# Optimization experiments

Hardware: AMD Instinct MI355X
Metric: run time of the kernel (lower is better)

The kernel has to match this reference:

```python
import jax, jax.numpy as jnp
import numpy as np

IN_F = 4096
OUT_F = 4096
R = 128
E = 8            # expert_num
R_PER = R // E   # per-expert low rank (16)
ALPHA = 16
SCALING = ALPHA / R
N = 8192


def setup_inputs() -> dict:
    key = jax.random.key(0)
    k_x, k_w0, k_g, k_a, k_b = jax.random.split(key, 5)
    x = jax.random.normal(k_x, (N, IN_F), dtype=jnp.float32)
    W0 = jax.random.normal(k_w0, (OUT_F, IN_F), dtype=jnp.float32) * 0.02   # base_layer weight
    Wg = jax.random.normal(k_g, (E, IN_F), dtype=jnp.float32) * 0.02        # GateL weight
    A = jax.random.normal(k_a, (E, R_PER, IN_F), dtype=jnp.float32) * 0.01  # stacked loraA weights
    B = jax.random.normal(k_b, (E, OUT_F, R_PER), dtype=jnp.float32) * 0.01 # stacked loraB weights
    return {"x": x, "W0": W0, "Wg": Wg, "A": A, "B": B}


def reference(x, W0, Wg, A, B):
    # base layer: result = x @ W0^T
    result = jnp.einsum('nd,od->no', x, W0)
    # gate: softmax over experts (dim=1 for 2D input)
    gate = jax.nn.softmax(jnp.einsum('nd,ed->ne', x, Wg), axis=1)  # [N, E]
    # per-expert low-rank: h_i = x @ A_i^T ; y_i = h_i @ B_i^T
    h = jnp.einsum('nd,erd->ner', x, A)        # [N, E, R_PER]
    y = jnp.einsum('ner,eor->neo', h, B)       # [N, E, OUT_F]
    lora = jnp.einsum('neo,ne->no', y, gate)   # gated weighted sum over experts
    return result + SCALING * lora
```

## Files before the change

kernel.cpp:

```cpp
#include <hip/hip_runtime.h>
#include <hip/hip_bf16.h>

#define IN_F   4096
#define OUT_F  4096
#define RTOT   128
#define NE     8
#define RP     16
#define NROWS  8192
#define KC     (IN_F + RTOT)
#define NG     144
#define SCALING 0.125f
#define KSPLIT 4

typedef __attribute__((ext_vector_type(8))) short bf16x8;
typedef __attribute__((ext_vector_type(4))) float f32x4;

__device__ __forceinline__ void gl_lds16(const __hip_bfloat16* g, __hip_bfloat16* l) {
    __builtin_amdgcn_global_load_lds(
        (const __attribute__((address_space(1))) unsigned int*)g,
        (__attribute__((address_space(3))) unsigned int*)l, 16, 0, 0);
}

union bf8pack { bf16x8 v; __hip_bfloat16 h[8]; };
union bf4pack { ushort4 u; __hip_bfloat16 h[4]; };

#define PREP_GRID 33856
__global__ void k_prep(const float* __restrict__ W0, const float* __restrict__ B,
                       const float* __restrict__ A, const float* __restrict__ Wg,
                       const float* __restrict__ x,
                       __hip_bfloat16* __restrict__ Wcat, __hip_bfloat16* __restrict__ AG,
                       __hip_bfloat16* __restrict__ Xcat) {
    int bid = blockIdx.x, tid = threadIdx.x;
    if (bid < 16896) {
        int i4 = (bid * 256 + tid) * 4;
        int o = i4 / KC;
        int c = i4 - o * KC;
        float4 v;
        if (c < IN_F) v = *(const float4*)&W0[(size_t)o * IN_F + c];
        else {
            int k = c - IN_F, e = k >> 4, r = k & 15;
            v = *(const float4*)&B[(size_t)((e * OUT_F + o) << 4) + r];
        }
        bf4pack p;
        p.h[0] = __float2bfloat16(v.x); p.h[1] = __float2bfloat16(v.y);
        p.h[2] = __float2bfloat16(v.z); p.h[3] = __float2bfloat16(v.w);
        *(ushort4*)&Wcat[i4] = p.u;
    } else if (bid < 17472) {
        int j4 = ((bid - 16896) * 256 + tid) * 4;
        int row = j4 >> 12, d = j4 & 4095;
        float4 v = {0.f, 0.f, 0.f, 0.f};
        if (row < RTOT)      v = *(const float4*)&A[j4];
        else if (row < 136)  v = *(const float4*)&Wg[((row - RTOT) << 12) + d];
        bf4pack p;
        p.h[0] = __float2bfloat16(v.x); p.h[1] = __float2bfloat16(v.y);
        p.h[2] = __float2bfloat16(v.z); p.h[3] = __float2bfloat16(v.w);
        *(ushort4*)&AG[j4] = p.u;
    } else {
        int t = (bid - 17472) * 256 + tid;
        int n = t >> 9, c8 = t & 511;
        const float4* src = (const float4*)&x[((size_t)n << 12) + (c8 << 3)];
        float4 v0 = src[0], v1 = src[1];
        bf8pack p;
        p.h[0] = __float2bfloat16(v0.x); p.h[1] = __float2bfloat16(v0.y);
        p.h[2] = __float2bfloat16(v0.z); p.h[3] = __float2bfloat16(v0.w);
        p.h[4] = __float2bfloat16(v1.x); p.h[5] = __float2bfloat16(v1.y);
        p.h[6] = __float2bfloat16(v1.z); p.h[7] = __float2bfloat16(v1.w);
        *(bf16x8*)&Xcat[(size_t)n * KC + (c8 << 3)] = p.v;
    }
}

__global__ __launch_bounds__(256) void k_hgemm(const __hip_bfloat16* __restrict__ Xcat,
                                               const __hip_bfloat16* __restrict__ AG,
                                               float* __restrict__ H) {
    __shared__ __hip_bfloat16 sX[128 * 32];
    __shared__ __hip_bfloat16 sG[NG * 32];
    const int tid  = threadIdx.x;
    const int lane = tid & 63;
    const int w    = tid >> 6;
    const int quad = lane >> 4;
    const int l16  = lane & 15;
    const int m0   = blockIdx.x * 128;
    const int kbeg = blockIdx.y * (IN_F / KSPLIT);

    f32x4 acc[2][9];
    for (int i = 0; i < 2; ++i)
        for (int j = 0; j < 9; ++j)
            acc[i][j] = (f32x4){0.f, 0.f, 0.f, 0.f};

    const int sr = tid >> 2;
    const int sk2 = (((tid & 3) ^ ((sr >> 1) & 3)) << 3);
    const int qq  = quad ^ ((l16 >> 1) & 3);

    for (int kt = kbeg; kt < kbeg + IN_F / KSPLIT; kt += 32) {
        __syncthreads();
        gl_lds16(&Xcat[(size_t)(m0 + sr) * KC + kt + sk2],      &sX[tid * 8]);
        gl_lds16(&Xcat[(size_t)(m0 + 64 + sr) * KC + kt + sk2], &sX[(tid + 256) * 8]);
        gl_lds16(&AG[(size_t)sr * IN_F + kt + sk2],             &sG[tid * 8]);
        gl_lds16(&AG[(size_t)(64 + sr) * IN_F + kt + sk2],      &sG[(tid + 256) * 8]);
        if (tid < 64)
            gl_lds16(&AG[(size_t)(128 + sr) * IN_F + kt + sk2], &sG[(tid + 512) * 8]);
        __syncthreads();

        bf16x8 a[2], b[9];
#pragma unroll
        for (int ti = 0; ti < 2; ++ti)
            a[ti] = *(const bf16x8*)(&sX[(w * 32 + ti * 16 + l16) * 32 + qq * 8]);
#pragma unroll
        for (int tj = 0; tj < 9; ++tj)
            b[tj] = *(const bf16x8*)(&sG[(tj * 16 + l16) * 32 + qq * 8]);
#pragma unroll
        for (int ti = 0; ti < 2; ++ti)
#pragma unroll
            for (int tj = 0; tj < 9; ++tj)
                acc[ti][tj] = __builtin_amdgcn_mfma_f32_16x16x32_bf16(a[ti], b[tj], acc[ti][tj], 0, 0, 0);
    }

    float* Hs = &H[(size_t)blockIdx.y * NROWS * NG];
#pragma unroll
    for (int ti = 0; ti < 2; ++ti)
#pragma unroll
        for (int tj = 0; tj < 9; ++tj) {
            int col = tj * 16 + l16;
#pragma unroll
            for (int i = 0; i < 4; ++i) {
                int row = m0 + w * 32 + ti * 16 + quad * 4 + i;
                Hs[(size_t)row * NG + col] = acc[ti][tj][i];
            }
        }
}

__global__ void k_gate(const float* __restrict__ H, __hip_bfloat16* __restrict__ Xcat) {
    int id = blockIdx.x * 256 + threadIdx.x;
    int n = id >> 4, k8 = id & 15;
    const float* hb = &H[(size_t)n * NG];
    float lg[NE] = {0.f, 0.f, 0.f, 0.f, 0.f, 0.f, 0.f, 0.f};
#pragma unroll
    for (int s = 0; s < KSPLIT; ++s) {
        const float* hs = hb + (size_t)s * NROWS * NG;
        float4 g0 = *(const float4*)&hs[128];
        float4 g1 = *(const float4*)&hs[132];
        lg[0] += g0.x; lg[1] += g0.y; lg[2] += g0.z; lg[3] += g0.w;
        lg[4] += g1.x; lg[5] += g1.y; lg[6] += g1.z; lg[7] += g1.w;
    }
    float mx = lg[0];
#pragma unroll
    for (int e = 1; e < NE; ++e) mx = fmaxf(mx, lg[e]);
    float ssum = 0.f;
#pragma unroll
    for (int e = 0; e < NE; ++e) { lg[e] = __expf(lg[e] - mx); ssum += lg[e]; }
    float inv = SCALING / ssum;
    int e = k8 >> 1;
    float ge = 0.f;
#pragma unroll
    for (int e2 = 0; e2 < NE; ++e2) if (e2 == e) ge = lg[e2];
    ge *= inv;
    float hv[8] = {0.f, 0.f, 0.f, 0.f, 0.f, 0.f, 0.f, 0.f};
#pragma unroll
    for (int s = 0; s < KSPLIT; ++s) {
        const float* hs = hb + (size_t)s * NROWS * NG;
        float4 h0 = *(const float4*)&hs[k8 * 8];
        float4 h1 = *(const float4*)&hs[k8 * 8 + 4];
        hv[0] += h0.x; hv[1] += h0.y; hv[2] += h0.z; hv[3] += h0.w;
        hv[4] += h1.x; hv[5] += h1.y; hv[6] += h1.z; hv[7] += h1.w;
    }
    bf8pack p;
#pragma unroll
    for (int i = 0; i < 8; ++i) p.h[i] = __float2bfloat16(hv[i] * ge);
    *(bf16x8*)&Xcat[(size_t)n * KC + IN_F + k8 * 8] = p.v;
}


#define BARRIER() __builtin_amdgcn_s_barrier()
#define SBAR()    __builtin_amdgcn_sched_barrier(0)
#define LGKM0()   do { asm volatile("s_waitcnt lgkmcnt(0)" ::: "memory"); SBAR(); } while (0)
#define VMCNT6()  asm volatile("s_waitcnt vmcnt(6)" ::: "memory")
#define VMCNT0()  asm volatile("s_waitcnt vmcnt(0)" ::: "memory")
#define PRIO(x)   __builtin_amdgcn_s_setprio(x)

#define STAGE(buf, op, half, koff) do {                                               \
        const __hip_bfloat16* _g = ((op) ? gB : gA) + (size_t)(half) * 128 * KC + (koff); \
        __hip_bfloat16* _l = lds + ((buf) * 4 + (op) * 2 + (half)) * 8192 + tid * 8;  \
        gl_lds16(_g, _l);                                                             \
        gl_lds16(_g + (size_t)64 * KC, _l + 4096);                                    \
    } while (0)

#define DS_A(b, mbase) do {                                                           \
        _Pragma("unroll") for (int mi = 0; mi < 4; ++mi) {                            \
            const __hip_bfloat16* _p = As[b] + (((mbase) + mi) * 16 + l16) * 64;      \
            a[mi][0] = *(const bf16x8*)(_p + kc0);                                    \
            a[mi][1] = *(const bf16x8*)(_p + kc1);                                    \
        } } while (0)

#define DS_B(b, dst, nbase) do {                                                      \
        _Pragma("unroll") for (int nj = 0; nj < 2; ++nj) {                            \
            const __hip_bfloat16* _p = Bs[b] + (brow0 + ((nbase) + nj) * 16 + l16) * 64; \
            dst[nj][0] = *(const bf16x8*)(_p + kc0);                                  \
            dst[nj][1] = *(const bf16x8*)(_p + kc1);                                  \
        } } while (0)

#define MM(mb, dst, nb) do {                                                          \
        _Pragma("unroll") for (int mi = 0; mi < 4; ++mi)                              \
        _Pragma("unroll") for (int nj = 0; nj < 2; ++nj) {                            \
            acc[(mb) + mi][(nb) + nj] = __builtin_amdgcn_mfma_f32_16x16x32_bf16(      \
                a[mi][0], dst[nj][0], acc[(mb) + mi][(nb) + nj], 0, 0, 0);            \
            acc[(mb) + mi][(nb) + nj] = __builtin_amdgcn_mfma_f32_16x16x32_bf16(      \
                a[mi][1], dst[nj][1], acc[(mb) + mi][(nb) + nj], 0, 0, 0);            \
        } } while (0)

__global__ __launch_bounds__(512, 2) void k_gemm(const __hip_bfloat16* __restrict__ Xcat,
                                                 const __hip_bfloat16* __restrict__ Wcat,
                                                 float* __restrict__ out) {
    __shared__ __hip_bfloat16 lds[8 * 8192];
    const int tid  = threadIdx.x;
    const int lane = tid & 63;
    const int w    = tid >> 6;
    const int wm   = w >> 2, wn = w & 3;
    const int quad = lane >> 4;
    const int l16  = lane & 15;
    const int xr   = l16 & 7;

    const int bid = blockIdx.x;
    const int swz = (bid & 7) * 64 + (bid >> 3);
    const int m0  = (swz >> 4) * 256;
    const int n0  = (swz & 15) * 256;

    const int srow = tid >> 3;
    const int scol = ((tid & 7) ^ (srow & 7)) << 3;
    const __hip_bfloat16* gA = Xcat + (size_t)(m0 + srow) * KC + scol;
    const __hip_bfloat16* gB = Wcat + (size_t)(n0 + srow) * KC + scol;

    const __hip_bfloat16* As[2] = { lds + (0 + wm) * 8192,        lds + (4 + wm) * 8192 };
    const __hip_bfloat16* Bs[2] = { lds + (2 + (wn >> 1)) * 8192, lds + (6 + (wn >> 1)) * 8192 };
    const int brow0 = (wn & 1) * 64;
    const int kc0 = (quad ^ xr) * 8;
    const int kc1 = ((4 + quad) ^ xr) * 8;

    f32x4 acc[8][4];
#pragma unroll
    for (int i = 0; i < 8; ++i)
#pragma unroll
        for (int j = 0; j < 4; ++j)
            acc[i][j] = (f32x4){0.f, 0.f, 0.f, 0.f};
    bf16x8 a[4][2], bl[2][2], bh[2][2];

    STAGE(0, 1, 0, 0);
    STAGE(0, 1, 1, 0);
    STAGE(0, 0, 0, 0);
    STAGE(0, 0, 1, 0);
    STAGE(1, 1, 0, 64);
    STAGE(1, 1, 1, 64);
    STAGE(1, 0, 0, 64);
    VMCNT6();
    BARRIER(); SBAR();

#pragma unroll 1
    for (int i = 0; i < 33; ++i) {
        const int kb    = i * 128;
        const int t1off = kb + 64;
        const int s0off = (kb + 128 <= KC - 64) ? kb + 128 : KC - 64;
        const int s1off = (kb + 192 <= KC - 64) ? kb + 192 : KC - 64;

        DS_A(0, 0); DS_B(0, bl, 0);
        STAGE(1, 0, 1, t1off);
        BARRIER(); LGKM0();
        PRIO(1); MM(0, bl, 0); PRIO(0);
        BARRIER(); SBAR();

        DS_B(0, bh, 2);
        BARRIER(); LGKM0();
        PRIO(1); MM(0, bh, 2); PRIO(0);
        BARRIER(); SBAR();

        DS_A(0, 4);
        STAGE(0, 1, 0, s0off);
        STAGE(0, 1, 1, s0off);
        BARRIER(); LGKM0();
        PRIO(1); MM(4, bh, 2); PRIO(0);
        BARRIER(); SBAR();

        STAGE(0, 0, 0, s0off);
        BARRIER(); LGKM0();
        PRIO(1); MM(4, bl, 0); PRIO(0);
        VMCNT6();
        BARRIER(); SBAR();

        DS_A(1, 0); DS_B(1, bl, 0);
        STAGE(0, 0, 1, s0off);
        BARRIER(); LGKM0();
        PRIO(1); MM(0, bl, 0); PRIO(0);
        BARRIER(); SBAR();

        DS_B(1, bh, 2);
        BARRIER(); LGKM0();
        PRIO(1); MM(0, bh, 2); PRIO(0);
        BARRIER(); SBAR();

        DS_A(1, 4);
        STAGE(1, 1, 0, s1off);
        STAGE(1, 1, 1, s1off);
        BARRIER(); LGKM0();
        PRIO(1); MM(4, bh, 2); PRIO(0);
        BARRIER(); SBAR();

        STAGE(1, 0, 0, s1off);
        BARRIER(); LGKM0();
        PRIO(1); MM(4, bl, 0); PRIO(0);
        VMCNT6();
        BARRIER(); SBAR();
    }
    VMCNT0();

#pragma unroll
    for (int ti = 0; ti < 8; ++ti)
#pragma unroll
        for (int tj = 0; tj < 4; ++tj) {
            int col = n0 + wn * 64 + tj * 16 + l16;
#pragma unroll
            for (int r = 0; r < 4; ++r) {
                int row = m0 + wm * 128 + ti * 16 + quad * 4 + r;
                out[(size_t)row * OUT_F + col] = acc[ti][tj][r];
            }
        }
}

extern "C" void kernel_launch(void* const* d_in, const int* in_sizes, int n_in,
                              void* d_out, int out_size, void* d_ws, size_t ws_size,
                              hipStream_t stream) {
    const float* x  = (const float*)d_in[0];
    const float* W0 = (const float*)d_in[1];
    const float* Wg = (const float*)d_in[2];
    const float* A  = (const float*)d_in[3];
    const float* B  = (const float*)d_in[4];
    float* out = (float*)d_out;

    char* ws = (char*)d_ws;
    size_t off = 0;
    __hip_bfloat16* Xcat = (__hip_bfloat16*)(ws + off); off += (size_t)NROWS * KC * 2;
    __hip_bfloat16* Wcat = (__hip_bfloat16*)(ws + off); off += (size_t)OUT_F * KC * 2;
    __hip_bfloat16* AG   = (__hip_bfloat16*)(ws + off); off += (size_t)NG * IN_F * 2;
    float*          H    = (float*)(ws + off);          off += (size_t)KSPLIT * NROWS * NG * 4;

    k_prep<<<PREP_GRID, 256, 0, stream>>>(W0, B, A, Wg, x, Wcat, AG, Xcat);
    k_hgemm<<<dim3(NROWS / 128, KSPLIT), 256, 0, stream>>>(Xcat, AG, H);
    k_gate<<<(NROWS * 16) / 256, 256, 0, stream>>>(H, Xcat);
    k_gemm<<<512, 512, 0, stream>>>(Xcat, Wcat, out);
}
```

Before: 522.1 us.

## Halve hgemm row tile and respread main GEMM staging across MFMA phases

The small gate/lora-A GEMM now uses 64-row tiles instead of 128, doubling its grid to 512 blocks for better CU occupancy at the cost of reloading the AG tile twice as often. In the main GEMM, the prologue issues one less stage and each of the eight MFMA phases now carries exactly one STAGE load, with the wait relaxed to vmcnt(4). This spreads global->LDS traffic evenly across compute phases but shortens the prefetch distance for some tiles, which risks stalls or a race if the wait counts are off.

```diff
diff --git a/kernel.cpp b/kernel.cpp
--- a/kernel.cpp
+++ b/kernel.cpp
@@ -72,20 +72,18 @@
 __global__ __launch_bounds__(256) void k_hgemm(const __hip_bfloat16* __restrict__ Xcat,
                                                const __hip_bfloat16* __restrict__ AG,
                                                float* __restrict__ H) {
-    __shared__ __hip_bfloat16 sX[128 * 32];
+    __shared__ __hip_bfloat16 sX[64 * 32];
     __shared__ __hip_bfloat16 sG[NG * 32];
     const int tid  = threadIdx.x;
     const int lane = tid & 63;
     const int w    = tid >> 6;
     const int quad = lane >> 4;
     const int l16  = lane & 15;
-    const int m0   = blockIdx.x * 128;
+    const int m0   = blockIdx.x * 64;
     const int kbeg = blockIdx.y * (IN_F / KSPLIT);
 
-    f32x4 acc[2][9];
-    for (int i = 0; i < 2; ++i)
-        for (int j = 0; j < 9; ++j)
-            acc[i][j] = (f32x4){0.f, 0.f, 0.f, 0.f};
+    f32x4 acc[9];
+    for (int j = 0; j < 9; ++j) acc[j] = (f32x4){0.f, 0.f, 0.f, 0.f};
 
     const int sr = tid >> 2;
     const int sk2 = (((tid & 3) ^ ((sr >> 1) & 3)) << 3);
@@ -94,39 +92,32 @@
     for (int kt = kbeg; kt < kbeg + IN_F / KSPLIT; kt += 32) {
         __syncthreads();
         gl_lds16(&Xcat[(size_t)(m0 + sr) * KC + kt + sk2],      &sX[tid * 8]);
-        gl_lds16(&Xcat[(size_t)(m0 + 64 + sr) * KC + kt + sk2], &sX[(tid + 256) * 8]);
         gl_lds16(&AG[(size_t)sr * IN_F + kt + sk2],             &sG[tid * 8]);
         gl_lds16(&AG[(size_t)(64 + sr) * IN_F + kt + sk2],      &sG[(tid + 256) * 8]);
         if (tid < 64)
             gl_lds16(&AG[(size_t)(128 + sr) * IN_F + kt + sk2], &sG[(tid + 512) * 8]);
         __syncthreads();
 
-        bf16x8 a[2], b[9];
-#pragma unroll
-        for (int ti = 0; ti < 2; ++ti)
-            a[ti] = *(const bf16x8*)(&sX[(w * 32 + ti * 16 + l16) * 32 + qq * 8]);
+        bf16x8 a = *(const bf16x8*)(&sX[(w * 16 + l16) * 32 + qq * 8]);
+        bf16x8 b[9];
 #pragma unroll
         for (int tj = 0; tj < 9; ++tj)
             b[tj] = *(const bf16x8*)(&sG[(tj * 16 + l16) * 32 + qq * 8]);
 #pragma unroll
-        for (int ti = 0; ti < 2; ++ti)
-#pragma unroll
-            for (int tj = 0; tj < 9; ++tj)
-                acc[ti][tj] = __builtin_amdgcn_mfma_f32_16x16x32_bf16(a[ti], b[tj], acc[ti][tj], 0, 0, 0);
+        for (int tj = 0; tj < 9; ++tj)
+            acc[tj] = __builtin_amdgcn_mfma_f32_16x16x32_bf16(a, b[tj], acc[tj], 0, 0, 0);
     }
 
     float* Hs = &H[(size_t)blockIdx.y * NROWS * NG];
 #pragma unroll
-    for (int ti = 0; ti < 2; ++ti)
-#pragma unroll
-        for (int tj = 0; tj < 9; ++tj) {
-            int col = tj * 16 + l16;
-#pragma unroll
-            for (int i = 0; i < 4; ++i) {
-                int row = m0 + w * 32 + ti * 16 + quad * 4 + i;
-                Hs[(size_t)row * NG + col] = acc[ti][tj][i];
-            }
+    for (int tj = 0; tj < 9; ++tj) {
+        int col = tj * 16 + l16;
+#pragma unroll
+        for (int i = 0; i < 4; ++i) {
+            int row = m0 + w * 16 + quad * 4 + i;
+            Hs[(size_t)row * NG + col] = acc[tj][i];
         }
+    }
 }
 
 __global__ void k_gate(const float* __restrict__ H, __hip_bfloat16* __restrict__ Xcat) {
@@ -173,7 +164,7 @@
 #define BARRIER() __builtin_amdgcn_s_barrier()
 #define SBAR()    __builtin_amdgcn_sched_barrier(0)
 #define LGKM0()   do { asm volatile("s_waitcnt lgkmcnt(0)" ::: "memory"); SBAR(); } while (0)
-#define VMCNT6()  asm volatile("s_waitcnt vmcnt(6)" ::: "memory")
+#define VMCNT4()  asm volatile("s_waitcnt vmcnt(4)" ::: "memory")
 #define VMCNT0()  asm volatile("s_waitcnt vmcnt(0)" ::: "memory")
 #define PRIO(x)   __builtin_amdgcn_s_setprio(x)
 
@@ -249,8 +240,7 @@
     STAGE(0, 0, 1, 0);
     STAGE(1, 1, 0, 64);
     STAGE(1, 1, 1, 64);
-    STAGE(1, 0, 0, 64);
-    VMCNT6();
+    VMCNT4();
     BARRIER(); SBAR();
 
 #pragma unroll 1
@@ -261,51 +251,51 @@
         const int s1off = (kb + 192 <= KC - 64) ? kb + 192 : KC - 64;
 
         DS_A(0, 0); DS_B(0, bl, 0);
+        STAGE(1, 0, 0, t1off);
+        BARRIER(); LGKM0();
+        PRIO(1); MM(0, bl, 0); PRIO(0);
+        BARRIER(); SBAR();
+
+        DS_B(0, bh, 2);
         STAGE(1, 0, 1, t1off);
-        BARRIER(); LGKM0();
-        PRIO(1); MM(0, bl, 0); PRIO(0);
-        BARRIER(); SBAR();
-
-        DS_B(0, bh, 2);
         BARRIER(); LGKM0();
         PRIO(1); MM(0, bh, 2); PRIO(0);
         BARRIER(); SBAR();
 
         DS_A(0, 4);
         STAGE(0, 1, 0, s0off);
+        BARRIER(); LGKM0();
+        PRIO(1); MM(4, bh, 2); PRIO(0);
+        BARRIER(); SBAR();
+
         STAGE(0, 1, 1, s0off);
         BARRIER(); LGKM0();
-        PRIO(1); MM(4, bh, 2); PRIO(0);
-        BARRIER(); SBAR();
-
+        PRIO(1); MM(4, bl, 0); PRIO(0);
+        VMCNT4();
+        BARRIER(); SBAR();
+
+        DS_A(1, 0); DS_B(1, bl, 0);
         STAGE(0, 0, 0, s0off);
         BARRIER(); LGKM0();
-        PRIO(1); MM(4, bl, 0); PRIO(0);
-        VMCNT6();
-        BARRIER(); SBAR();
-
-        DS_A(1, 0); DS_B(1, bl, 0);
+        PRIO(1); MM(0, bl, 0); PRIO(0);
+        BARRIER(); SBAR();
+
+        DS_B(1, bh, 2);
         STAGE(0, 0, 1, s0off);
-        BARRIER(); LGKM0();
-        PRIO(1); MM(0, bl, 0); PRIO(0);
-        BARRIER(); SBAR();
-
-        DS_B(1, bh, 2);
         BARRIER(); LGKM0();
         PRIO(1); MM(0, bh, 2); PRIO(0);
         BARRIER(); SBAR();
 
         DS_A(1, 4);
         STAGE(1, 1, 0, s1off);
+        BARRIER(); LGKM0();
+        PRIO(1); MM(4, bh, 2); PRIO(0);
+        BARRIER(); SBAR();
+
         STAGE(1, 1, 1, s1off);
         BARRIER(); LGKM0();
-        PRIO(1); MM(4, bh, 2); PRIO(0);
-        BARRIER(); SBAR();
-
-        STAGE(1, 0, 0, s1off);
-        BARRIER(); LGKM0();
         PRIO(1); MM(4, bl, 0); PRIO(0);
-        VMCNT6();
+        VMCNT4();
         BARRIER(); SBAR();
     }
     VMCNT0();
@@ -341,7 +331,7 @@
     float*          H    = (float*)(ws + off);          off += (size_t)KSPLIT * NROWS * NG * 4;
 
     k_prep<<<PREP_GRID, 256, 0, stream>>>(W0, B, A, Wg, x, Wcat, AG, Xcat);
-    k_hgemm<<<dim3(NROWS / 128, KSPLIT), 256, 0, stream>>>(Xcat, AG, H);
+    k_hgemm<<<dim3(NROWS / 64, KSPLIT), 256, 0, stream>>>(Xcat, AG, H);
     k_gate<<<(NROWS * 16) / 256, 256, 0, stream>>>(H, Xcat);
     k_gemm<<<512, 512, 0, stream>>>(Xcat, Wcat, out);
 }
```

Result: faster. 510.6 us (-2.2%).
